# Kernel optimization log

Hardware: AMD Instinct MI355X
Metric: run time of the kernel (lower is better)

## Reference

```python
import jax, jax.numpy as jnp
import numpy as np

DEPTH = 10
LAMDA = 1e-3

def setup_inputs() -> dict:
    key = jax.random.key(0)
    k1, k2, k3 = jax.random.split(key, 3)
    B, D = 32768, 784
    n_internal = 2 ** DEPTH - 1  # 1023
    n_leaf = 2 ** DEPTH          # 1024
    out_dim = 10
    X = jax.random.normal(k1, (B, D), dtype=jnp.float32)
    W_inner = jax.random.normal(k2, (n_internal, D + 1), dtype=jnp.float32) * 0.05
    W_leaf = jax.random.normal(k3, (out_dim, n_leaf), dtype=jnp.float32) * 0.05
    return {"X": X, "W_inner": W_inner, "W_leaf": W_leaf}

def reference(X, W_inner, W_leaf):
    B = X.shape[0]
    dtype = X.dtype
    # data augment: prepend constant-1 bias column -> [B, D+1]
    Xa = jnp.concatenate([jnp.ones((B, 1), dtype), X], axis=1)
    # inner nodes: linear (no bias) + sigmoid -> [B, n_internal]
    p = jax.nn.sigmoid(Xa @ W_inner.T)
    # left/right routing probs -> [B, n_internal, 2]
    path_prob = jnp.stack([p, 1.0 - p], axis=2)
    mu = jnp.ones((B, 1), dtype)  # path prob to each node at current layer
    penalty = jnp.zeros((), dtype)
    begin = 0
    for layer_idx in range(DEPTH):
        n = 2 ** layer_idx
        pp = path_prob[:, begin:begin + n, :].reshape(B, 2 * n)  # [B, 2n]
        mu_rep = jnp.repeat(mu, 2, axis=1)  # parent prob for node j is mu[:, j//2]
        # alpha_j = sum_b pp[:, j] * mu_parent[:, j] / sum_b mu_parent[:, j]
        alpha = jnp.sum(pp * mu_rep, axis=0) / jnp.sum(mu_rep, axis=0)
        coeff = LAMDA * 2.0 ** (-layer_idx)
        penalty = penalty - 0.5 * coeff * jnp.sum(jnp.log(alpha) + jnp.log(1.0 - alpha))
        mu = mu_rep * pp  # [B, 2n]
        begin += n
    # mu is [B, 2^DEPTH]; leaf linear (no bias)
    y_pred = mu @ W_leaf.T  # [B, out_dim]
    return y_pred, penalty
```

## Files before the change

kernel.cpp:

```cpp
#include <hip/hip_runtime.h>
#include <stdint.h>


#define BROWS 32768
#define KDIM  784
#define NNODE 1023
#define NP    1024
#define NLEAF 1024
#define OUTD  10
#define NDEPTH 10
#define LAMDA 1e-3f
#define NBKT  32

#define GKS   800
#define GKW   800
#define NT    25
#define BUFS  12288

typedef __attribute__((ext_vector_type(8))) short short8;
typedef __attribute__((ext_vector_type(4))) float f32x4;

__device__ __forceinline__ unsigned short f2bf(float f) {
    unsigned int u = __float_as_uint(f);
    u = u + 0x7FFFu + ((u >> 16) & 1u);
    return (unsigned short)(u >> 16);
}
__device__ __forceinline__ float bf2f(unsigned short h) {
    return __uint_as_float(((unsigned int)h) << 16);
}

__global__ __launch_bounds__(256)
void sdt_xsplit(const float* __restrict__ X, unsigned short* __restrict__ Xs)
{
    const int g   = blockIdx.x * 256 + threadIdx.x;
    const int row = g / 100, grp = g % 100;
    unsigned int hi[4];
    if (grp < 98) {
        const float4* src = reinterpret_cast<const float4*>(&X[(size_t)row * KDIM + grp * 8]);
        const float4 v0 = src[0], v1 = src[1];
        const float v[8] = {v0.x, v0.y, v0.z, v0.w, v1.x, v1.y, v1.z, v1.w};
#pragma unroll
        for (int i = 0; i < 4; ++i)
            hi[i] = (unsigned int)f2bf(v[2*i]) | ((unsigned int)f2bf(v[2*i+1]) << 16);
    } else {
#pragma unroll
        for (int i = 0; i < 4; ++i) hi[i] = 0u;
    }
    *reinterpret_cast<uint4*>(&Xs[(size_t)row * GKS + grp * 8]) = make_uint4(hi[0], hi[1], hi[2], hi[3]);
}

__global__ __launch_bounds__(256)
void sdt_wsplit(const float* __restrict__ Wi, unsigned short* __restrict__ Ws,
                float* __restrict__ bias)
{
    const int row = blockIdx.x;
    const int tid = threadIdx.x;
    for (int c = tid; c < GKW; c += 256) {
        unsigned short v = 0;
        if (row < NNODE && c < KDIM) v = f2bf(Wi[(size_t)row * (KDIM + 1) + 1 + c]);
        Ws[(size_t)row * GKW + c] = v;
    }
    if (tid == 0) bias[row] = (row < NNODE) ? Wi[(size_t)row * (KDIM + 1)] : 0.f;
}

#define BAR() { __builtin_amdgcn_sched_barrier(0); __builtin_amdgcn_s_barrier(); __builtin_amdgcn_sched_barrier(0); }

#define STAGE(ktn, sel)                                                               \
    {                                                                                 \
        const int kt_ = (ktn);                                                        \
        const int kk_ = kt_ * 32;                                                     \
        unsigned short* ab_ = lds + (sel) * BUFS;                                     \
        unsigned short* bb_ = ab_ + 4096;                                             \
        __builtin_amdgcn_global_load_lds(                                             \
            (const __attribute__((address_space(1))) void*)(pA + kk_),                \
            (__attribute__((address_space(3))) void*)(ab_ + (wave * 64) * 8),         \
            16, 0, 0);                                                                \
        _Pragma("unroll")                                                             \
        for (int j = 0; j < 2; ++j)                                                   \
            __builtin_amdgcn_global_load_lds(                                         \
                (const __attribute__((address_space(1))) void*)(pB[j] + kk_),         \
                (__attribute__((address_space(3))) void*)(bb_ + (j * 512 + wave * 64) * 8), \
                16, 0, 0);                                                            \
    }

#define LDA4(dst, ab_)                                                                \
    _Pragma("unroll")                                                                 \
    for (int mi = 0; mi < 4; ++mi) {                                                  \
        const int row_ = wr * 64 + mi * 16 + fr;                                      \
        dst[mi] = *reinterpret_cast<const short8*>(                                   \
            (ab_) + row_ * 32 + ((q4 ^ ((row_ >> 1) & 3)) * 8));                      \
    }

#define LDB4(dst, bb_)                                                                \
    _Pragma("unroll")                                                                 \
    for (int n = 0; n < 4; ++n) {                                                     \
        const int row_ = wc * 64 + n * 16 + fr;                                       \
        dst[n] = *reinterpret_cast<const short8*>(                                    \
            (bb_) + row_ * 32 + ((q4 ^ ((row_ >> 1) & 3)) * 8));                      \
    }

#define MFMA16(av, bv)                                                                \
    _Pragma("unroll")                                                                 \
    for (int mi = 0; mi < 4; ++mi)                                                    \
        _Pragma("unroll")                                                             \
        for (int n = 0; n < 4; ++n)                                                   \
            acc[mi][n] = __builtin_amdgcn_mfma_f32_16x16x32_bf16(                     \
                av[mi], bv[n], acc[mi][n], 0, 0, 0);

__global__ __launch_bounds__(512, 4)
void sdt_gemm8(const unsigned short* __restrict__ Xs, const unsigned short* __restrict__ Ws,
               const float* __restrict__ bias, unsigned short* __restrict__ P)
{
    __shared__ __align__(16) unsigned short lds[36864];

    const int tid  = threadIdx.x;
    const int wave = tid >> 6, lane = tid & 63;
    const int wr = wave >> 2, wc = wave & 3;
    const int b  = blockIdx.x;
    const int wg = (b & 7) * 128 + (b >> 3);
    const int col0 = (wg & 3) * 256;
    const int row0 = (wg >> 2) * 128;

    const int fr = lane & 15;
    const int q4 = lane >> 4;

    f32x4 acc[4][4];
#pragma unroll
    for (int i = 0; i < 4; ++i)
#pragma unroll
        for (int j = 0; j < 4; ++j) acc[i][j] = (f32x4)0.f;

    const unsigned short* pA;
    {
        const int r = tid >> 2;
        const int kc = (tid & 3) ^ ((r >> 1) & 3);
        pA = Xs + (size_t)(row0 + r) * GKS + kc * 8;
    }
    const unsigned short* pB[2];
#pragma unroll
    for (int j = 0; j < 2; ++j) {
        const int c = j * 512 + tid;
        const int r = c >> 2;
        const int kc = (c & 3) ^ ((r >> 1) & 3);
        pB[j] = Ws + (size_t)(col0 + r) * GKW + kc * 8;
    }

    STAGE(0, 0);
    STAGE(1, 1);

#pragma unroll 1
    for (int kt = 0; kt < NT; ++kt) {
        if (kt < NT - 1) { asm volatile("s_waitcnt vmcnt(3)" ::: "memory"); }
        else             { asm volatile("s_waitcnt vmcnt(0)" ::: "memory"); }
        BAR();
        const int cs = kt % 3;
        const unsigned short* ab = lds + cs * BUFS;
        const unsigned short* bb = ab + 4096;
        short8 a[4], bfr[4];
        LDA4(a, ab);
        LDB4(bfr, bb);
        if (kt + 2 < NT) STAGE(kt + 2, (kt + 2) % 3);
        __builtin_amdgcn_s_setprio(1);
        MFMA16(a, bfr);
        __builtin_amdgcn_s_setprio(0);
    }

    __syncthreads();
    unsigned short* tr = lds + wave * 4096;
    float bv[4];
#pragma unroll
    for (int n = 0; n < 4; ++n) bv[n] = bias[col0 + wc * 64 + n * 16 + fr];

#pragma unroll
    for (int m = 0; m < 4; ++m)
#pragma unroll
        for (int reg = 0; reg < 4; ++reg) {
            const int rl = m * 16 + q4 * 4 + reg;
#pragma unroll
            for (int n = 0; n < 4; ++n) {
                const float z = acc[m][n][reg] + bv[n];
                const float p = 1.f / (1.f + __expf(-z));
                tr[rl * 64 + n * 16 + fr] = f2bf(p);
            }
        }
#pragma unroll
    for (int it = 0; it < 8; ++it) {
        const int r  = it * 8 + (lane >> 3);
        const int c8 = (lane & 7) * 8;
        const uint4 v = *reinterpret_cast<const uint4*>(tr + r * 64 + c8);
        *reinterpret_cast<uint4*>(
            &P[(size_t)(row0 + wr * 64 + r) * NP + col0 + wc * 64 + c8]) = v;
    }
}

__global__ __launch_bounds__(256)
void sdt_tree(const unsigned short* __restrict__ P, const float* __restrict__ Wl,
              float* __restrict__ Y, float* __restrict__ leafsum32)
{
    __shared__ float rd[4][2][832];
    __shared__ float lsb[4][1024];
    const int tid = threadIdx.x;
    const int wave = tid >> 6, lane = tid & 63;

    float lsum[16];
#pragma unroll
    for (int i = 0; i < 16; ++i) lsum[i] = 0.f;

    float4 wreg[OUTD][4];
#pragma unroll
    for (int o = 0; o < OUTD; ++o)
#pragma unroll
        for (int i4 = 0; i4 < 4; ++i4)
            wreg[o][i4] = *reinterpret_cast<const float4*>(
                &Wl[o * NLEAF + lane * 16 + i4 * 4]);

    const int rowbase = blockIdx.x * 32 + wave * 8;
    const int o_r   = lane % 10;
    const int seg16 = (lane / 10) * 16;

#pragma unroll 2
    for (int r = 0; r < 8; ++r) {
        const int row = rowbase + r;
        const unsigned short* pr = P + (size_t)row * NP;
        float* rw = rd[wave][r & 1];

        const float preg = bf2f(pr[lane]);

        float mu = 1.f; int f = 0;
#pragma unroll
        for (int d = 0; d < 6; ++d) {
            const int bit = (lane >> (5 - d)) & 1;
            const float pv = __shfl(preg, f, 64);
            mu *= bit ? (1.f - pv) : pv;
            f = 2 * f + 1 + bit;
        }

        const float p6 = bf2f(pr[63 + lane]);
        float m1[2];
        m1[0] = mu * p6; m1[1] = mu * (1.f - p6);

        const unsigned int u7 = *reinterpret_cast<const unsigned int*>(pr + 128 + 2 * lane);
        const float lo7 = bf2f((unsigned short)(u7 & 0xffffu));
        const float hi7 = bf2f((unsigned short)(u7 >> 16));
        float e7 = __shfl_up(hi7, 1, 64);
        if (lane == 0) e7 = bf2f(pr[127]);
        float m2[4];
        m2[0] = m1[0] * e7;  m2[1] = m1[0] * (1.f - e7);
        m2[2] = m1[1] * lo7; m2[3] = m1[1] * (1.f - lo7);

        const uint2 u8 = *reinterpret_cast<const uint2*>(pr + 256 + 4 * lane);
        const float a0 = bf2f((unsigned short)(u8.x & 0xffffu));
        const float a1 = bf2f((unsigned short)(u8.x >> 16));
        const float a2 = bf2f((unsigned short)(u8.y & 0xffffu));
        const float a3 = bf2f((unsigned short)(u8.y >> 16));
        float e8 = __shfl_up(a3, 1, 64);
        if (lane == 0) e8 = bf2f(pr[255]);
        const float p8v[4] = {e8, a0, a1, a2};
        float m3[8];
#pragma unroll
        for (int i = 0; i < 4; ++i) {
            m3[2 * i] = m2[i] * p8v[i]; m3[2 * i + 1] = m2[i] * (1.f - p8v[i]);
        }

        const uint4 u9 = *reinterpret_cast<const uint4*>(pr + 512 + 8 * lane);
        const float b0 = bf2f((unsigned short)(u9.x & 0xffffu));
        const float b1 = bf2f((unsigned short)(u9.x >> 16));
        const float b2 = bf2f((unsigned short)(u9.y & 0xffffu));
        const float b3 = bf2f((unsigned short)(u9.y >> 16));
        const float b4 = bf2f((unsigned short)(u9.z & 0xffffu));
        const float b5 = bf2f((unsigned short)(u9.z >> 16));
        const float b6 = bf2f((unsigned short)(u9.w & 0xffffu));
        const float b7 = bf2f((unsigned short)(u9.w >> 16));
        float e9 = __shfl_up(b7, 1, 64);
        if (lane == 0) e9 = bf2f(pr[511]);
        const float p9v[8] = {e9, b0, b1, b2, b3, b4, b5, b6};
        float m4[16];
#pragma unroll
        for (int i = 0; i < 8; ++i) {
            m4[2 * i] = m3[i] * p9v[i]; m4[2 * i + 1] = m3[i] * (1.f - p9v[i]);
        }
#pragma unroll
        for (int i = 0; i < 16; ++i) lsum[i] += m4[i];

#pragma unroll
        for (int o = 0; o < OUTD; ++o) {
            float s = 0.f;
#pragma unroll
            for (int i4 = 0; i4 < 4; ++i4) {
                const float4 w4 = wreg[o][i4];
                s = fmaf(m4[4 * i4 + 0], w4.x, s);
                s = fmaf(m4[4 * i4 + 1], w4.y, s);
                s = fmaf(m4[4 * i4 + 2], w4.z, s);
                s = fmaf(m4[4 * i4 + 3], w4.w, s);
            }
            rw[lane * 13 + o] = s;
        }
        float s = 0.f;
        if (lane < 40) {
#pragma unroll
            for (int m = 0; m < 16; ++m) s += rw[(seg16 + m) * 13 + o_r];
        }
        s += __shfl_down(s, 20, 64);
        s += __shfl_down(s, 10, 64);
        if (lane < 10) Y[(size_t)row * OUTD + lane] = s;
    }

#pragma unroll
    for (int i = 0; i < 16; ++i) {
        const int ii = (i + lane) & 15;
        lsb[wave][lane * 16 + ii] = lsum[ii];
    }
    __syncthreads();
    float* bkt = leafsum32 + (size_t)(blockIdx.x & (NBKT - 1)) * NLEAF;
    for (int idx = tid; idx < NLEAF; idx += 256) {
        const float s = lsb[0][idx] + lsb[1][idx] + lsb[2][idx] + lsb[3][idx];
        atomicAdd(&bkt[idx], s);
    }
}

__global__ __launch_bounds__(1024)
void sdt_penalty(const float* __restrict__ leafsum32, float* __restrict__ pen_out)
{
    __shared__ float t[NLEAF];
    __shared__ float red1[1024];
    const int tid = threadIdx.x;
    float accv = 0.f;
#pragma unroll
    for (int k = 0; k < NBKT; ++k) accv += leafsum32[k * NLEAF + tid];
    t[tid] = accv;
    __syncthreads();
    float pen = 0.f;
    for (int d = NDEPTH; d >= 1; --d) {
        const int n = 1 << d;
        if (tid < n) {
            const float num = t[tid];
            const float par = t[tid & ~1] + t[tid | 1];
            const float a = num / par;
            const float coeff = LAMDA * exp2f((float)(1 - d));
            pen -= 0.5f * coeff * (logf(a) + logf(1.f - a));
        }
        float s = 0.f;
        if (tid < (n >> 1)) s = t[2 * tid] + t[2 * tid + 1];
        __syncthreads();
        if (tid < (n >> 1)) t[tid] = s;
        __syncthreads();
    }
    red1[tid] = pen;
    __syncthreads();
    for (int off = 512; off >= 1; off >>= 1) {
        if (tid < off) red1[tid] += red1[tid + off];
        __syncthreads();
    }
    if (tid == 0) pen_out[0] = red1[0];
}

extern "C" void kernel_launch(void* const* d_in, const int* in_sizes, int n_in,
                              void* d_out, int out_size, void* d_ws, size_t ws_size,
                              hipStream_t stream)
{
    const float* X  = (const float*)d_in[0];
    const float* Wi = (const float*)d_in[1];
    const float* Wl = (const float*)d_in[2];
    float* Y   = (float*)d_out;
    float* pen = Y + (size_t)BROWS * OUTD;

    char* ws = (char*)d_ws;
    const size_t P_BYTES  = (size_t)BROWS * NP * 2;
    const size_t XS_BYTES = (size_t)BROWS * GKS * 2;
    const size_t WS_BYTES = (size_t)NP * GKW * 2;

    unsigned short* P   = (unsigned short*)ws;
    unsigned short* Xs  = (unsigned short*)(ws + P_BYTES);
    unsigned short* Wsp = (unsigned short*)(ws + P_BYTES + XS_BYTES);
    float* bias      = (float*)(ws + P_BYTES + XS_BYTES + WS_BYTES);
    float* leafsum32 = (float*)(ws + P_BYTES + XS_BYTES + WS_BYTES + 4096);

    hipMemsetAsync(leafsum32, 0, NBKT * NLEAF * sizeof(float), stream);
    sdt_xsplit<<<BROWS * 100 / 256, 256, 0, stream>>>(X, Xs);
    sdt_wsplit<<<1024, 256, 0, stream>>>(Wi, Wsp, bias);
    sdt_gemm8<<<1024, 512, 0, stream>>>(Xs, Wsp, bias, P);
    sdt_tree<<<BROWS / 32, 256, 0, stream>>>(P, Wl, Y, leafsum32);
    sdt_penalty<<<1, 1024, 0, stream>>>(leafsum32, pen);
}
```

Before: 155.4 us.

## Fuse fp32-to-bf16 conversion of X into the GEMM A-tile load path

Removes the separate X conversion kernel. The GEMM now loads fp32 X rows into registers, packs them to bf16 and writes them into the swizzled LDS A buffer, one stage ahead through register double-buffering. The B tiles keep using direct global-to-LDS loads, and the wait counts and barrier placement are reorganised around the new pipeline. This avoids writing and re-reading an intermediate bf16 copy of X and one kernel launch. In exchange, each GEMM block reads twice as many bytes of A, since the data is now fp32. Padded K columns are clamped to valid addresses and rely on the zero-padded weights.

```diff
diff --git a/kernel.cpp b/kernel.cpp
--- a/kernel.cpp
+++ b/kernel.cpp
@@ -1,4 +1,5 @@
 #include <hip/hip_runtime.h>
+#include <hip/hip_bf16.h>
 #include <stdint.h>
 
 
@@ -12,7 +13,6 @@
 #define LAMDA 1e-3f
 #define NBKT  32
 
-#define GKS   800
 #define GKW   800
 #define NT    25
 #define BUFS  12288
@@ -28,25 +28,9 @@
 __device__ __forceinline__ float bf2f(unsigned short h) {
     return __uint_as_float(((unsigned int)h) << 16);
 }
-
-__global__ __launch_bounds__(256)
-void sdt_xsplit(const float* __restrict__ X, unsigned short* __restrict__ Xs)
-{
-    const int g   = blockIdx.x * 256 + threadIdx.x;
-    const int row = g / 100, grp = g % 100;
-    unsigned int hi[4];
-    if (grp < 98) {
-        const float4* src = reinterpret_cast<const float4*>(&X[(size_t)row * KDIM + grp * 8]);
-        const float4 v0 = src[0], v1 = src[1];
-        const float v[8] = {v0.x, v0.y, v0.z, v0.w, v1.x, v1.y, v1.z, v1.w};
-#pragma unroll
-        for (int i = 0; i < 4; ++i)
-            hi[i] = (unsigned int)f2bf(v[2*i]) | ((unsigned int)f2bf(v[2*i+1]) << 16);
-    } else {
-#pragma unroll
-        for (int i = 0; i < 4; ++i) hi[i] = 0u;
-    }
-    *reinterpret_cast<uint4*>(&Xs[(size_t)row * GKS + grp * 8]) = make_uint4(hi[0], hi[1], hi[2], hi[3]);
+__device__ __forceinline__ unsigned int pk2bf(float a, float b) {
+    __hip_bfloat162 h = __float22bfloat162_rn(make_float2(a, b));
+    return *reinterpret_cast<unsigned int*>(&h);
 }
 
 __global__ __launch_bounds__(256)
@@ -65,22 +49,35 @@
 
 #define BAR() { __builtin_amdgcn_sched_barrier(0); __builtin_amdgcn_s_barrier(); __builtin_amdgcn_sched_barrier(0); }
 
-#define STAGE(ktn, sel)                                                               \
+#define STAGE_B(ktn, sel)                                                             \
     {                                                                                 \
-        const int kt_ = (ktn);                                                        \
-        const int kk_ = kt_ * 32;                                                     \
-        unsigned short* ab_ = lds + (sel) * BUFS;                                     \
-        unsigned short* bb_ = ab_ + 4096;                                             \
-        __builtin_amdgcn_global_load_lds(                                             \
-            (const __attribute__((address_space(1))) void*)(pA + kk_),                \
-            (__attribute__((address_space(3))) void*)(ab_ + (wave * 64) * 8),         \
-            16, 0, 0);                                                                \
+        const int kk_ = (ktn) * 32;                                                   \
+        unsigned short* bb_ = lds + (sel) * BUFS + 4096;                              \
         _Pragma("unroll")                                                             \
         for (int j = 0; j < 2; ++j)                                                   \
             __builtin_amdgcn_global_load_lds(                                         \
                 (const __attribute__((address_space(1))) void*)(pB[j] + kk_),         \
                 (__attribute__((address_space(3))) void*)(bb_ + (j * 512 + wave * 64) * 8), \
                 16, 0, 0);                                                            \
+    }
+
+#define ALOAD(ktn, d0, d1)                                                            \
+    {                                                                                 \
+        const int ca0_ = (ktn) * 32 + kcA * 8;                                        \
+        const int cb0_ = ca0_ + 4;                                                    \
+        const int ca_ = (ca0_ >= KDIM) ? 0 : ca0_;                                    \
+        const int cb_ = (cb0_ >= KDIM) ? 0 : cb0_;                                    \
+        d0 = *reinterpret_cast<const float4*>(pXrow + ca_);                           \
+        d1 = *reinterpret_cast<const float4*>(pXrow + cb_);                           \
+    }
+
+#define AWRITE(sel, d0, d1)                                                           \
+    {                                                                                 \
+        unsigned short* ab_ = lds + (sel) * BUFS;                                     \
+        union { short8 s; unsigned int u[4]; } t_;                                    \
+        t_.u[0] = pk2bf(d0.x, d0.y); t_.u[1] = pk2bf(d0.z, d0.w);                     \
+        t_.u[2] = pk2bf(d1.x, d1.y); t_.u[3] = pk2bf(d1.z, d1.w);                     \
+        *reinterpret_cast<short8*>(ab_ + tid * 8) = t_.s;                             \
     }
 
 #define LDA4(dst, ab_)                                                                \
@@ -108,7 +105,7 @@
                 av[mi], bv[n], acc[mi][n], 0, 0, 0);
 
 __global__ __launch_bounds__(512, 4)
-void sdt_gemm8(const unsigned short* __restrict__ Xs, const unsigned short* __restrict__ Ws,
+void sdt_gemm8(const float* __restrict__ X, const unsigned short* __restrict__ Ws,
                const float* __restrict__ bias, unsigned short* __restrict__ P)
 {
     __shared__ __align__(16) unsigned short lds[36864];
@@ -130,12 +127,10 @@
 #pragma unroll
         for (int j = 0; j < 4; ++j) acc[i][j] = (f32x4)0.f;
 
-    const unsigned short* pA;
-    {
-        const int r = tid >> 2;
-        const int kc = (tid & 3) ^ ((r >> 1) & 3);
-        pA = Xs + (size_t)(row0 + r) * GKS + kc * 8;
-    }
+    const int rA  = tid >> 2;
+    const int kcA = (tid & 3) ^ ((rA >> 1) & 3);
+    const float* pXrow = X + (size_t)(row0 + rA) * KDIM;
+
     const unsigned short* pB[2];
 #pragma unroll
     for (int j = 0; j < 2; ++j) {
@@ -145,24 +140,36 @@
         pB[j] = Ws + (size_t)(col0 + r) * GKW + kc * 8;
     }
 
-    STAGE(0, 0);
-    STAGE(1, 1);
+    float4 ac0, ac1, an0, an1;
+    ALOAD(0, ac0, ac1);
+    ALOAD(1, an0, an1);
+    STAGE_B(0, 0);
+    STAGE_B(1, 1);
+    AWRITE(0, ac0, ac1);
+    ac0 = an0; ac1 = an1;
+    asm volatile("s_waitcnt vmcnt(2) lgkmcnt(0)" ::: "memory");
+    BAR();
 
 #pragma unroll 1
     for (int kt = 0; kt < NT; ++kt) {
-        if (kt < NT - 1) { asm volatile("s_waitcnt vmcnt(3)" ::: "memory"); }
-        else             { asm volatile("s_waitcnt vmcnt(0)" ::: "memory"); }
-        BAR();
         const int cs = kt % 3;
         const unsigned short* ab = lds + cs * BUFS;
         const unsigned short* bb = ab + 4096;
         short8 a[4], bfr[4];
         LDA4(a, ab);
         LDB4(bfr, bb);
-        if (kt + 2 < NT) STAGE(kt + 2, (kt + 2) % 3);
+        if (kt + 1 < NT) AWRITE((kt + 1) % 3, ac0, ac1);
+        if (kt + 2 < NT) {
+            ALOAD(kt + 2, an0, an1);
+            STAGE_B(kt + 2, (kt + 2) % 3);
+        }
+        ac0 = an0; ac1 = an1;
         __builtin_amdgcn_s_setprio(1);
         MFMA16(a, bfr);
         __builtin_amdgcn_s_setprio(0);
+        if (kt < NT - 3) { asm volatile("s_waitcnt vmcnt(4) lgkmcnt(0)" ::: "memory"); }
+        else             { asm volatile("s_waitcnt vmcnt(0) lgkmcnt(0)" ::: "memory"); }
+        BAR();
     }
 
     __syncthreads();
@@ -366,19 +373,16 @@
 
     char* ws = (char*)d_ws;
     const size_t P_BYTES  = (size_t)BROWS * NP * 2;
-    const size_t XS_BYTES = (size_t)BROWS * GKS * 2;
     const size_t WS_BYTES = (size_t)NP * GKW * 2;
 
     unsigned short* P   = (unsigned short*)ws;
-    unsigned short* Xs  = (unsigned short*)(ws + P_BYTES);
-    unsigned short* Wsp = (unsigned short*)(ws + P_BYTES + XS_BYTES);
-    float* bias      = (float*)(ws + P_BYTES + XS_BYTES + WS_BYTES);
-    float* leafsum32 = (float*)(ws + P_BYTES + XS_BYTES + WS_BYTES + 4096);
+    unsigned short* Wsp = (unsigned short*)(ws + P_BYTES);
+    float* bias      = (float*)(ws + P_BYTES + WS_BYTES);
+    float* leafsum32 = (float*)(ws + P_BYTES + WS_BYTES + 4096);
 
     hipMemsetAsync(leafsum32, 0, NBKT * NLEAF * sizeof(float), stream);
-    sdt_xsplit<<<BROWS * 100 / 256, 256, 0, stream>>>(X, Xs);
     sdt_wsplit<<<1024, 256, 0, stream>>>(Wi, Wsp, bias);
-    sdt_gemm8<<<1024, 512, 0, stream>>>(Xs, Wsp, bias, P);
+    sdt_gemm8<<<1024, 512, 0, stream>>>(X, Wsp, bias, P);
     sdt_tree<<<BROWS / 32, 256, 0, stream>>>(P, Wl, Y, leafsum32);
     sdt_penalty<<<1, 1024, 0, stream>>>(leafsum32, pen);
 }
```

Result: faster. 143.5 us (-7.7%).
